# Kernel tuning notes

Hardware: AMD Instinct MI355X
Metric: run time of the kernel (lower is better)

Reference implementation:

```python
import jax, jax.numpy as jnp
import numpy as np

B, L = 8, 1024
VOCAB = 5000
DW = 256            # d_word_vec = d_model
H = 3 * DW          # hidden_size = 768
NH, HD = 12, 64     # n_head, d_k
D = NH * HD         # 768 = nhead*head_dim
D_INNER = 3072
N_LAYERS = 2
N_HIDDEN = 1024
N_OUT = 5000
MASK = 0
SCALE = 1.0 / float(np.sqrt(HD))


def _sinusoid(n_pos, d_hid):
    pos = np.arange(n_pos, dtype=np.float64)[:, None]
    hid = np.arange(d_hid)[None, :]
    tab = pos / np.power(10000.0, 2 * (hid // 2) / d_hid)
    tab[:, 0::2] = np.sin(tab[:, 0::2])
    tab[:, 1::2] = np.cos(tab[:, 1::2])
    tab[0] = 0.0  # padding_idx=0
    return jnp.asarray(tab, dtype=jnp.float32)


def _ln(x, g, b, eps=1e-5):
    mu = x.mean(-1, keepdims=True)
    var = ((x - mu) ** 2).mean(-1, keepdims=True)
    return (x - mu) * jax.lax.rsqrt(var + eps) * g + b


def _dense(x, w, b):
    # w: [out, in] (torch Conv 1x1 / Linear convention)
    return jnp.einsum('...i,oi->...o', x, w) + b


def _pwff(x, w1, b1, w2, b2, g, bn):
    out = _dense(jax.nn.relu(_dense(x, w1, b1)), w2, b2)
    return _ln(out + x, g, bn)


def _msa1(x, relay, wq, bq, wk, bk, wv, bv, wo, bo):
    # x: [B, L, H] nodes, relay: [B, H]. Star-Transformer ring attention:
    # window = 3 local neighbors + the relay node (4 keys per query).
    Bx, Lx, _ = x.shape
    q = _dense(x, wq, bq).reshape(Bx, Lx, NH, HD)
    k = _dense(x, wk, bk).reshape(Bx, Lx, NH, HD)
    v = _dense(x, wv, bv).reshape(Bx, Lx, NH, HD)
    kp = jnp.pad(k, ((0, 0), (1, 1), (0, 0), (0, 0)))
    vp = jnp.pad(v, ((0, 0), (1, 1), (0, 0), (0, 0)))
    k_win = jnp.stack([kp[:, u:u + Lx] for u in range(3)], axis=2)  # [B,L,3,NH,HD]
    v_win = jnp.stack([vp[:, u:u + Lx] for u in range(3)], axis=2)
    rk = _dense(relay, wk, bk).reshape(Bx, NH, HD)
    rv = _dense(relay, wv, bv).reshape(Bx, NH, HD)
    s_loc = jnp.einsum('blnh,blwnh->blwn', q, k_win)
    s_rel = jnp.einsum('blnh,bnh->bln', q, rk)
    scores = jnp.concatenate([s_loc, s_rel[:, :, None, :]], axis=2) * SCALE  # [B,L,4,NH]
    a = jax.nn.softmax(scores, axis=2)
    att = jnp.einsum('blwn,blwnh->blnh', a[:, :, :3], v_win) + a[:, :, 3][..., None] * rv[:, None]
    return _dense(att.reshape(Bx, Lx, D), wo, bo)


def _msa2(relay, nodes, smask, wq, bq, wk, bk, wv, bv, wo, bo):
    # Satellite->planet global attention: single query (relay) over [relay; nodes].
    Bx = relay.shape[0]
    y = jnp.concatenate([relay[:, None, :], nodes], axis=1)  # [B, 1+L, H]
    q = _dense(relay, wq, bq).reshape(Bx, NH, HD)
    k = _dense(y, wk, bk).reshape(Bx, -1, NH, HD)
    v = _dense(y, wv, bv).reshape(Bx, -1, NH, HD)
    pre = jnp.einsum('bnh,bsnh->bns', q, k) * SCALE
    pre = jnp.where(smask[:, None, :], -jnp.inf, pre)
    a = jax.nn.softmax(pre, axis=2)
    att = jnp.einsum('bns,bsnh->bnh', a, v).reshape(Bx, D)
    return _dense(att, wo, bo)


def setup_inputs():
    ks = iter(jax.random.split(jax.random.key(0), 40))
    def w(shape):
        return jax.random.normal(next(ks), shape, dtype=jnp.float32) * 0.02
    def z(shape):
        return jnp.zeros(shape, jnp.float32)
    def o(shape):
        return jnp.ones(shape, jnp.float32)
    inp = {}
    inp['src_seq'] = jax.random.randint(next(ks), (B, L, 3), 0, VOCAB, dtype=jnp.int32)
    inp['positions'] = jax.random.randint(next(ks), (B,), 0, L, dtype=jnp.int32)
    inp['emb'] = w((VOCAB, DW))
    inp['pos_table'] = _sinusoid(L, H)
    inp['norm_g'] = o((N_LAYERS, H)); inp['norm_b'] = z((N_LAYERS, H))
    inp['pw_w1'] = w((N_LAYERS, D_INNER, H)); inp['pw_b1'] = z((N_LAYERS, D_INNER))
    inp['pw_w2'] = w((N_LAYERS, H, D_INNER)); inp['pw_b2'] = z((N_LAYERS, H))
    inp['pw_g'] = o((N_LAYERS, H)); inp['pw_bn'] = z((N_LAYERS, H))
    for p in ['ring', 'star']:
        inp[p + '_wq'] = w((N_LAYERS, D, H)); inp[p + '_bq'] = z((N_LAYERS, D))
        inp[p + '_wk'] = w((N_LAYERS, D, H)); inp[p + '_bk'] = z((N_LAYERS, D))
        inp[p + '_wv'] = w((N_LAYERS, D, H)); inp[p + '_bv'] = z((N_LAYERS, D))
        inp[p + '_wo'] = w((N_LAYERS, H, D)); inp[p + '_bo'] = z((N_LAYERS, H))
    inp['head_w1'] = w((3, N_HIDDEN, 2 * H)); inp['head_b1'] = z((3, N_HIDDEN))
    inp['head_w2'] = w((3, N_OUT, N_HIDDEN)); inp['head_b2'] = z((3, N_OUT))
    return inp


def reference(src_seq, positions, emb, pos_table, norm_g, norm_b, pw_w1, pw_b1, pw_w2, pw_b2, pw_g, pw_bn, ring_wq, ring_bq, ring_wk, ring_bk, ring_wv, ring_bv, ring_wo, ring_bo, star_wq, star_bq, star_wk, star_bk, star_wv, star_bv, star_wo, star_bo, head_w1, head_b1, head_w2, head_b2):
    Bx, Lx, _ = src_seq.shape
    # [B,L,3,DW] -> [B,L,H], add (frozen) sinusoid positional encoding
    x = emb[src_seq].reshape(Bx, Lx, H) + pos_table[None, :Lx]
    mask_pad = src_seq[:, :, 0] == MASK               # True at padded positions
    smask = jnp.concatenate([jnp.zeros((Bx, 1), bool), mask_pad], axis=1)
    nodes = x
    relay = x.mean(axis=1)                            # [B, H]
    for i in range(N_LAYERS):
        h = _pwff(nodes, pw_w1[i], pw_b1[i], pw_w2[i], pw_b2[i], pw_g[i], pw_bn[i])
        ring = _msa1(h, relay, ring_wq[i], ring_bq[i], ring_wk[i], ring_bk[i], ring_wv[i], ring_bv[i], ring_wo[i], ring_bo[i])
        nodes = jax.nn.leaky_relu(_ln(ring, norm_g[i], norm_b[i]))
        relay = jax.nn.leaky_relu(_msa2(relay, nodes, smask, star_wq[i], star_bq[i], star_wk[i], star_bk[i], star_wv[i], star_bv[i], star_wo[i], star_bo[i]))
        nodes = jnp.where(mask_pad[:, :, None], 0.0, nodes)
    target = nodes[jnp.arange(Bx), positions]         # [B, H]
    ft = jnp.concatenate([relay, target], axis=1)     # [B, 2H]
    outs = [_dense(jax.nn.relu(_dense(ft, head_w1[j], head_b1[j])), head_w2[j], head_b2[j]) for j in range(3)]
    return jnp.concatenate(outs, axis=1).reshape(3 * Bx, N_OUT)
```

## Files before the change

kernel.cpp:

```cpp
#include <hip/hip_runtime.h>
#include <cstdint>
#include <cstddef>


typedef unsigned short u16;
typedef __attribute__((ext_vector_type(4))) float f32x4;
typedef __attribute__((ext_vector_type(8))) __bf16 bf16x8;

#define NB 8
#define SEQ 1024
#define HDIM 768
#define NHEAD 12
#define HD 64
#define DINNER 3072
#define NHID 1024
#define NOUT 5000
#define ATT_SCALE 0.125f

static __device__ __forceinline__ float b2f(u16 u) {
  union { float f; uint32_t i; } v; v.i = ((uint32_t)u) << 16; return v.f;
}
static __device__ __forceinline__ u16 f2b(float f) {
  union { float f; uint32_t i; } v; v.f = f;
  uint32_t r = v.i + 0x7fffu + ((v.i >> 16) & 1u);
  return (u16)(r >> 16);
}
static __device__ __forceinline__ float2 b2f2(uint32_t u) {
  union { float f; uint32_t i; } lo, hi;
  lo.i = u << 16; hi.i = u & 0xffff0000u;
  return make_float2(lo.f, hi.f);
}

static __device__ __forceinline__ void gl2lds16(const void* g, void* l) {
  __builtin_amdgcn_global_load_lds(
      (__attribute__((address_space(1))) void*)(uintptr_t)g,
      (__attribute__((address_space(3))) void*)l, 16, 0, 0);
}

template <int N>
static __device__ __forceinline__ void wait_vmcnt() {
  if constexpr (N == 0) asm volatile("s_waitcnt vmcnt(0)" ::: "memory");
  else if constexpr (N == 3) asm volatile("s_waitcnt vmcnt(3)" ::: "memory");
  else if constexpr (N == 4) asm volatile("s_waitcnt vmcnt(4)" ::: "memory");
  else if constexpr (N == 6) asm volatile("s_waitcnt vmcnt(6)" ::: "memory");
  else if constexpr (N == 8) asm volatile("s_waitcnt vmcnt(8)" ::: "memory");
}

static __device__ __forceinline__ float blk_sum(float v, float* red) {
  #pragma unroll
  for (int off = 32; off > 0; off >>= 1) v += __shfl_down(v, off, 64);
  if ((threadIdx.x & 63) == 0) red[threadIdx.x >> 6] = v;
  __syncthreads();
  float r = red[0] + red[1] + red[2] + red[3];
  __syncthreads();
  return r;
}
static __device__ __forceinline__ float blk_max(float v, float* red) {
  #pragma unroll
  for (int off = 32; off > 0; off >>= 1) v = fmaxf(v, __shfl_down(v, off, 64));
  if ((threadIdx.x & 63) == 0) red[threadIdx.x >> 6] = v;
  __syncthreads();
  float r = fmaxf(fmaxf(red[0], red[1]), fmaxf(red[2], red[3]));
  __syncthreads();
  return r;
}

struct Cvt4 {
  const float* s0; const float* s1; const float* s2; const float* s3;
  u16* d0; u16* d1; u16* d2; u16* d3;
  int c1, c2, c3, c4;
};
__global__ __launch_bounds__(256) void cvt4_k(Cvt4 a) {
  const int i = blockIdx.x * 256 + threadIdx.x;
  if (i >= a.c4) return;
  const float* s; u16* d; int j;
  if (i < a.c1)      { s = a.s0; d = a.d0; j = i; }
  else if (i < a.c2) { s = a.s1; d = a.d1; j = i - a.c1; }
  else if (i < a.c3) { s = a.s2; d = a.d2; j = i - a.c2; }
  else               { s = a.s3; d = a.d3; j = i - a.c3; }
  const float4 v = ((const float4*)s)[j];
  ushort4 o;
  o.x = f2b(v.x); o.y = f2b(v.y); o.z = f2b(v.z); o.w = f2b(v.w);
  ((ushort4*)d)[j] = o;
}

template <int ACT, int TM>
__global__ __launch_bounds__(256) void gemm_bt(
    const u16* __restrict__ A,
    const u16* W0, const u16* W1, const u16* W2,
    const float* b0, const float* b1, const float* b2,
    u16* C0, u16* C1, u16* C2,
    int M, int N, int K) {
  constexpr int MI = TM / 32;
  constexpr int S = TM / 64 + 2;
  __shared__ u16 As[4][TM * 32];
  __shared__ u16 Bs[4][128 * 32];
  const int z = blockIdx.z;
  const u16* W = z == 0 ? W0 : (z == 1 ? W1 : W2);
  const float* bias = z == 0 ? b0 : (z == 1 ? b1 : b2);
  u16* C = z == 0 ? C0 : (z == 1 ? C1 : C2);

  const int tid  = threadIdx.x;
  const int wave = tid >> 6;
  const int lane = tid & 63;
  const int bm = blockIdx.y * TM;
  const int bn = blockIdx.x * 128;
  const int wrq = wave >> 1, wcq = wave & 1;
  const int r16 = lane & 15, quad = lane >> 4;
  const int srow = lane >> 2;
  const int scol = (lane & 3) << 3;

  f32x4 acc[MI][4] = {};

  const int nk = K >> 5;

  auto STAGE = [&](int s, int t) {
    const int k0 = t << 5;
    #pragma unroll
    for (int q = 0; q < TM / 64; ++q) {
      const int rowa = wave * (TM / 4) + q * 16;
      gl2lds16(A + (size_t)(bm + rowa + srow) * K + (k0 + scol),
               (char*)&As[s][0] + (rowa << 6));
    }
    #pragma unroll
    for (int q = 0; q < 2; ++q) {
      const int rowb = wave * 32 + q * 16;
      gl2lds16(W + (size_t)(bn + rowb + srow) * K + (k0 + scol),
               (char*)&Bs[s][0] + (rowb << 6));
    }
  };

  STAGE(0, 0);
  if (1 < nk) STAGE(1, 1);

  for (int t = 0; t < nk; ++t) {
    const int s = t & 3;
    if (t + 2 < nk) {
      STAGE((t + 2) & 3, t + 2);
      __builtin_amdgcn_sched_barrier(0);
      wait_vmcnt<2 * S>();
    } else if (t + 1 < nk) {
      wait_vmcnt<S>();
    } else {
      wait_vmcnt<0>();
    }
    __builtin_amdgcn_sched_barrier(0);
    __builtin_amdgcn_s_barrier();
    __builtin_amdgcn_sched_barrier(0);

    bf16x8 af[MI], bf[4];
    #pragma unroll
    for (int i = 0; i < MI; ++i)
      af[i] = *reinterpret_cast<const bf16x8*>(
          &As[s][(wrq * (TM / 2) + i * 16 + r16) * 32 + quad * 8]);
    #pragma unroll
    for (int j = 0; j < 4; ++j)
      bf[j] = *reinterpret_cast<const bf16x8*>(
          &Bs[s][(wcq * 64 + j * 16 + r16) * 32 + quad * 8]);
    #pragma unroll
    for (int i = 0; i < MI; ++i)
      #pragma unroll
      for (int j = 0; j < 4; ++j)
        acc[i][j] = __builtin_amdgcn_mfma_f32_16x16x32_bf16(af[i], bf[j], acc[i][j], 0, 0, 0);
  }

  #pragma unroll
  for (int j = 0; j < 4; ++j) {
    const int n = bn + wcq * 64 + j * 16 + r16;
    const float bv = bias[n];
    #pragma unroll
    for (int i = 0; i < MI; ++i) {
      const int m0 = bm + wrq * (TM / 2) + i * 16 + quad * 4;
      #pragma unroll
      for (int r = 0; r < 4; ++r) {
        float vv = acc[i][j][r] + bv;
        if (ACT == 1) vv = fmaxf(vv, 0.0f);
        C[(size_t)(m0 + r) * N + n] = f2b(vv);
      }
    }
  }
}

__global__ __launch_bounds__(256) void embed_k(
    const int* __restrict__ src, const float* __restrict__ emb,
    const float* __restrict__ pt, float* __restrict__ x,
    u16* __restrict__ xb) {
  const int r = blockIdx.x;
  const int l = r & (SEQ - 1);
  const int tid = threadIdx.x;
  #pragma unroll
  for (int it = 0; it < 3; ++it) {
    const int idx = tid + it * 256;
    const int c = idx >> 8, d = idx & 255;
    const int tok = src[r * 3 + c];
    const float v = emb[(size_t)tok * 256 + d] + pt[(size_t)l * HDIM + idx];
    x[(size_t)r * HDIM + idx] = v;
    xb[(size_t)r * HDIM + idx] = f2b(v);
  }
}

__global__ __launch_bounds__(256) void relay_mean1_k(
    const float* __restrict__ x, float* __restrict__ part) {
  const int cg = blockIdx.x, seg = blockIdx.y, b = blockIdx.z;
  const int h = cg * 256 + threadIdx.x;
  float s = 0.f;
  const int l0 = seg * 64;
  for (int l = l0; l < l0 + 64; ++l) s += x[((size_t)b * SEQ + l) * HDIM + h];
  part[((size_t)b * 16 + seg) * HDIM + h] = s;
}
__global__ __launch_bounds__(256) void relay_mean2_k(
    const float* __restrict__ part, float* __restrict__ relay) {
  const int b = blockIdx.y;
  const int h = blockIdx.x * 256 + threadIdx.x;
  float s = 0.f;
  #pragma unroll
  for (int i = 0; i < 16; ++i) s += part[((size_t)b * 16 + i) * HDIM + h];
  relay[b * HDIM + h] = s * (1.0f / 1024.0f);
}

__global__ __launch_bounds__(256) void ln_resid_k(
    const u16* __restrict__ pre, const float* __restrict__ res,
    const float* __restrict__ g, const float* __restrict__ bb,
    u16* __restrict__ out) {
  __shared__ float red[4];
  const int r = blockIdx.x;
  const int tid = threadIdx.x;
  const size_t base = (size_t)r * HDIM;
  float v0 = b2f(pre[base + tid])       + res[base + tid];
  float v1 = b2f(pre[base + tid + 256]) + res[base + tid + 256];
  float v2 = b2f(pre[base + tid + 512]) + res[base + tid + 512];
  const float mu = blk_sum(v0 + v1 + v2, red) * (1.0f / 768.0f);
  v0 -= mu; v1 -= mu; v2 -= mu;
  const float var = blk_sum(v0 * v0 + v1 * v1 + v2 * v2, red) * (1.0f / 768.0f);
  const float rs = rsqrtf(var + 1e-5f);
  out[base + tid]       = f2b(v0 * rs * g[tid]       + bb[tid]);
  out[base + tid + 256] = f2b(v1 * rs * g[tid + 256] + bb[tid + 256]);
  out[base + tid + 512] = f2b(v2 * rs * g[tid + 512] + bb[tid + 512]);
}

__global__ __launch_bounds__(256) void ln_leaky_mask_k(
    const u16* __restrict__ pre, const float* __restrict__ g,
    const float* __restrict__ bb, const int* __restrict__ src,
    float* __restrict__ out, u16* __restrict__ outb) {
  __shared__ float red[4];
  const int r = blockIdx.x;
  const int tid = threadIdx.x;
  const size_t base = (size_t)r * HDIM;
  float v0 = b2f(pre[base + tid]);
  float v1 = b2f(pre[base + tid + 256]);
  float v2 = b2f(pre[base + tid + 512]);
  const float mu = blk_sum(v0 + v1 + v2, red) * (1.0f / 768.0f);
  v0 -= mu; v1 -= mu; v2 -= mu;
  const float var = blk_sum(v0 * v0 + v1 * v1 + v2 * v2, red) * (1.0f / 768.0f);
  const float rs = rsqrtf(var + 1e-5f);
  const bool masked = (src[r * 3] == 0);
  float y0 = v0 * rs * g[tid]       + bb[tid];
  float y1 = v1 * rs * g[tid + 256] + bb[tid + 256];
  float y2 = v2 * rs * g[tid + 512] + bb[tid + 512];
  y0 = y0 > 0.f ? y0 : 0.01f * y0;
  y1 = y1 > 0.f ? y1 : 0.01f * y1;
  y2 = y2 > 0.f ? y2 : 0.01f * y2;
  if (masked) { y0 = 0.f; y1 = 0.f; y2 = 0.f; }
  out[base + tid]       = y0;  outb[base + tid]       = f2b(y0);
  out[base + tid + 256] = y1;  outb[base + tid + 256] = f2b(y1);
  out[base + tid + 512] = y2;  outb[base + tid + 512] = f2b(y2);
}

__global__ __launch_bounds__(256) void ring_attn_k(
    const u16* __restrict__ q, const u16* __restrict__ k,
    const u16* __restrict__ v, const float* __restrict__ rk,
    const float* __restrict__ rv, u16* __restrict__ att) {
  __shared__ float qs[HDIM];
  __shared__ float aw[NHEAD][4];
  const int r = blockIdx.x;
  const int b = r >> 10, l = r & (SEQ - 1);
  const int tid = threadIdx.x;
  const size_t base = (size_t)r * HDIM;
  #pragma unroll
  for (int it = 0; it < 3; ++it) {
    const int idx = tid + it * 256;
    qs[idx] = b2f(q[base + idx]);
  }
  __syncthreads();
  if (tid < 192) {
    const int u_ = tid >> 2;
    const int l4 = tid & 3;
    const int n = u_ >> 2, w = u_ & 3;
    const float* qrow = qs + n * HD + l4 * 16;
    float a = 0.f;
    if (w < 3) {
      const int ll = l - 1 + w;
      if (ll >= 0 && ll < SEQ) {
        const uint4* kp4 =
            (const uint4*)(k + base + (size_t)(w - 1) * HDIM + n * HD + l4 * 16);
        #pragma unroll
        for (int t = 0; t < 2; ++t) {
          const uint4 u = kp4[t];
          const float2 f0 = b2f2(u.x), f1 = b2f2(u.y);
          const float2 f2_ = b2f2(u.z), f3 = b2f2(u.w);
          const float* q8 = qrow + t * 8;
          a += q8[0] * f0.x + q8[1] * f0.y + q8[2] * f1.x + q8[3] * f1.y
             + q8[4] * f2_.x + q8[5] * f2_.y + q8[6] * f3.x + q8[7] * f3.y;
        }
      }
    } else {
      const float4* kp4 = (const float4*)(rk + b * HDIM + n * HD + l4 * 16);
      #pragma unroll
      for (int t = 0; t < 4; ++t) {
        const float4 kv = kp4[t];
        const float* q4 = qrow + t * 4;
        a += q4[0] * kv.x + q4[1] * kv.y + q4[2] * kv.z + q4[3] * kv.w;
      }
    }
    a += __shfl_xor(a, 1, 4);
    a += __shfl_xor(a, 2, 4);
    if (l4 == 0) aw[n][w] = a * ATT_SCALE;
  }
  __syncthreads();
  if (tid < NHEAD) {
    const float s0 = aw[tid][0], s1 = aw[tid][1], s2 = aw[tid][2], s3 = aw[tid][3];
    const float m = fmaxf(fmaxf(s0, s1), fmaxf(s2, s3));
    const float e0 = __expf(s0 - m), e1 = __expf(s1 - m);
    const float e2 = __expf(s2 - m), e3 = __expf(s3 - m);
    const float inv = 1.0f / (e0 + e1 + e2 + e3);
    aw[tid][0] = e0 * inv; aw[tid][1] = e1 * inv;
    aw[tid][2] = e2 * inv; aw[tid][3] = e3 * inv;
  }
  __syncthreads();
  #pragma unroll
  for (int it = 0; it < 3; ++it) {
    const int idx = tid + it * 256;
    const int n = idx >> 6;
    float acc = aw[n][3] * rv[b * HDIM + idx];
    if (l > 0)       acc += aw[n][0] * b2f(v[base - HDIM + idx]);
    acc += aw[n][1] * b2f(v[base + idx]);
    if (l < SEQ - 1) acc += aw[n][2] * b2f(v[base + HDIM + idx]);
    att[base + idx] = f2b(acc);
  }
}

__global__ __launch_bounds__(256) void msa2_attn_k(
    const float* __restrict__ q2, const float* __restrict__ rk2,
    const float* __restrict__ rv2, const u16* __restrict__ k2,
    const u16* __restrict__ v2, const int* __restrict__ src,
    float* __restrict__ att) {
  __shared__ float qs[HD];
  __shared__ float sc[SEQ + 1];
  __shared__ float red[4];
  __shared__ float vred[4][HD];
  const int bid = blockIdx.x;
  const int b = bid / NHEAD, n = bid % NHEAD;
  const int tid = threadIdx.x;
  const int hb = b * HDIM + n * HD;
  if (tid < HD) qs[tid] = q2[hb + tid];
  __syncthreads();
  float lmax = -1e30f;
  for (int s = tid; s <= SEQ; s += 256) {
    float sco;
    if (s == 0) {
      float a = 0.f;
      #pragma unroll
      for (int d = 0; d < HD; ++d) a += qs[d] * rk2[hb + d];
      sco = a * ATT_SCALE;
    } else {
      const int l = s - 1;
      if (src[(b * SEQ + l) * 3] == 0) {
        sco = -1e30f;
      } else {
        const uint4* kp4 =
            (const uint4*)(k2 + ((size_t)b * SEQ + l) * HDIM + n * HD);
        float a = 0.f;
        #pragma unroll
        for (int t = 0; t < 8; ++t) {
          const uint4 u = kp4[t];
          const float2 f0 = b2f2(u.x), f1 = b2f2(u.y);
          const float2 f2_ = b2f2(u.z), f3 = b2f2(u.w);
          const float* q8 = qs + t * 8;
          a += q8[0] * f0.x + q8[1] * f0.y + q8[2] * f1.x + q8[3] * f1.y
             + q8[4] * f2_.x + q8[5] * f2_.y + q8[6] * f3.x + q8[7] * f3.y;
        }
        sco = a * ATT_SCALE;
      }
    }
    sc[s] = sco;
    lmax = fmaxf(lmax, sco);
  }
  lmax = blk_max(lmax, red);
  float lsum = 0.f;
  for (int s = tid; s <= SEQ; s += 256) {
    const float e = __expf(sc[s] - lmax);
    sc[s] = e;
    lsum += e;
  }
  lsum = blk_sum(lsum, red);
  {
    const int dd = tid & 63, grp = tid >> 6;
    float acc = 0.f;
    const u16* vp = v2 + (size_t)b * SEQ * HDIM + n * HD + dd;
    for (int l = grp; l < SEQ; l += 4)
      acc += sc[l + 1] * b2f(vp[(size_t)l * HDIM]);
    vred[grp][dd] = acc;
  }
  __syncthreads();
  if (tid < HD) {
    const float inv = 1.0f / lsum;
    const float a = sc[0] * rv2[hb + tid]
                  + vred[0][tid] + vred[1][tid] + vred[2][tid] + vred[3][tid];
    att[hb + tid] = a * inv;
  }
}

__global__ __launch_bounds__(256) void relay_proj_k(
    const float* __restrict__ A, int N, int nm,
    const float* W0, const float* W1, const float* W2,
    const float* b0, const float* b1, const float* b2v,
    float* O0, float* O1, float* O2, int act) {
  const int wid = blockIdx.x * 4 + (threadIdx.x >> 6);
  const int lane = threadIdx.x & 63;
  const int mat = wid / N, n = wid % N;
  const float* W  = mat == 0 ? W0 : (mat == 1 ? W1 : W2);
  const float* bb = mat == 0 ? b0 : (mat == 1 ? b1 : b2v);
  float* O        = mat == 0 ? O0 : (mat == 1 ? O1 : O2);
  const float4* wr = (const float4*)(W + (size_t)n * HDIM);
  float acc[NB] = {};
  #pragma unroll
  for (int it = 0; it < 3; ++it) {
    const int k4 = it * 64 + lane;
    const float4 wv = wr[k4];
    #pragma unroll
    for (int b = 0; b < NB; ++b) {
      const float4 av = *(const float4*)&A[b * HDIM + k4 * 4];
      acc[b] += av.x * wv.x + av.y * wv.y + av.z * wv.z + av.w * wv.w;
    }
  }
  #pragma unroll
  for (int b = 0; b < NB; ++b) {
    float a = acc[b];
    #pragma unroll
    for (int off = 32; off > 0; off >>= 1) a += __shfl_down(a, off, 64);
    if (lane == 0) {
      float v = a + bb[n];
      if (act == 2) v = v > 0.f ? v : 0.01f * v;
      O[(size_t)b * N + n] = v;
    }
  }
}

__global__ __launch_bounds__(256) void ft_k(
    const float* __restrict__ relay, const float* __restrict__ nodes,
    const int* __restrict__ positions, float* __restrict__ ft) {
  const int gid = blockIdx.x * 256 + threadIdx.x;
  const int b = gid / 1536, j = gid % 1536;
  if (j < HDIM) {
    ft[gid] = relay[b * HDIM + j];
  } else {
    const int p = positions[b];
    ft[gid] = nodes[((size_t)b * SEQ + p) * HDIM + (j - HDIM)];
  }
}

__global__ __launch_bounds__(256) void head1_k(
    const float* __restrict__ ft, const float* __restrict__ w,
    const float* __restrict__ bias, float* __restrict__ hid) {
  __shared__ float fs[NB * 1536];
  const int j = blockIdx.y;
  {
    const float4* s4 = (const float4*)ft;
    float4* d4 = (float4*)fs;
    for (int i = threadIdx.x; i < (NB * 1536) / 4; i += 256) d4[i] = s4[i];
  }
  __syncthreads();
  const int wave = threadIdx.x >> 6, lane = threadIdx.x & 63;
  const int o = blockIdx.x * 4 + wave;
  const float4* wr = (const float4*)(w + ((size_t)j * NHID + o) * 1536);
  float acc[NB] = {};
  #pragma unroll
  for (int it = 0; it < 6; ++it) {
    const int k4 = it * 64 + lane;
    const float4 wv = wr[k4];
    #pragma unroll
    for (int b = 0; b < NB; ++b) {
      const float4 hv = *(const float4*)&fs[b * 1536 + k4 * 4];
      acc[b] += hv.x * wv.x + hv.y * wv.y + hv.z * wv.z + hv.w * wv.w;
    }
  }
  #pragma unroll
  for (int b = 0; b < NB; ++b) {
    float a = acc[b];
    #pragma unroll
    for (int off = 32; off > 0; off >>= 1) a += __shfl_down(a, off, 64);
    if (lane == 0)
      hid[((size_t)j * NB + b) * NHID + o] = fmaxf(a + bias[j * NHID + o], 0.f);
  }
}

__global__ __launch_bounds__(256) void head2_k(
    const float* __restrict__ hid, const float* __restrict__ w,
    const float* __restrict__ bias, float* __restrict__ out) {
  __shared__ float hs[NB * NHID];
  const int j = blockIdx.y;
  {
    const float4* s4 = (const float4*)(hid + (size_t)j * NB * NHID);
    float4* d4 = (float4*)hs;
    for (int i = threadIdx.x; i < (NB * NHID) / 4; i += 256) d4[i] = s4[i];
  }
  __syncthreads();
  const int wave = threadIdx.x >> 6, lane = threadIdx.x & 63;
  const int o = blockIdx.x * 4 + wave;
  const float4* wr = (const float4*)(w + ((size_t)j * NOUT + o) * NHID);
  float acc[NB] = {};
  #pragma unroll
  for (int it = 0; it < 4; ++it) {
    const int k4 = it * 64 + lane;
    const float4 wv = wr[k4];
    #pragma unroll
    for (int b = 0; b < NB; ++b) {
      const float4 hv = *(const float4*)&hs[b * NHID + k4 * 4];
      acc[b] += hv.x * wv.x + hv.y * wv.y + hv.z * wv.z + hv.w * wv.w;
    }
  }
  #pragma unroll
  for (int b = 0; b < NB; ++b) {
    float a = acc[b];
    #pragma unroll
    for (int off = 32; off > 0; off >>= 1) a += __shfl_down(a, off, 64);
    if (lane == 0)
      out[(size_t)(b * 3 + j) * NOUT + o] = a + bias[j * NOUT + o];
  }
}

extern "C" void kernel_launch(void* const* d_in, const int* in_sizes, int n_in,
                              void* d_out, int out_size, void* d_ws, size_t ws_size,
                              hipStream_t stream) {
  (void)in_sizes; (void)n_in; (void)out_size; (void)ws_size;
  const int* src       = (const int*)d_in[0];
  const int* positions = (const int*)d_in[1];
  const float* emb   = (const float*)d_in[2];
  const float* pt    = (const float*)d_in[3];
  const float* norm_g = (const float*)d_in[4]; const float* norm_b = (const float*)d_in[5];
  const float* pw_w1 = (const float*)d_in[6];  const float* pw_b1 = (const float*)d_in[7];
  const float* pw_w2 = (const float*)d_in[8];  const float* pw_b2 = (const float*)d_in[9];
  const float* pw_g  = (const float*)d_in[10]; const float* pw_bn = (const float*)d_in[11];
  const float* ring_wq = (const float*)d_in[12]; const float* ring_bq = (const float*)d_in[13];
  const float* ring_wk = (const float*)d_in[14]; const float* ring_bk = (const float*)d_in[15];
  const float* ring_wv = (const float*)d_in[16]; const float* ring_bv = (const float*)d_in[17];
  const float* ring_wo = (const float*)d_in[18]; const float* ring_bo = (const float*)d_in[19];
  const float* star_wq = (const float*)d_in[20]; const float* star_bq = (const float*)d_in[21];
  const float* star_wk = (const float*)d_in[22]; const float* star_bk = (const float*)d_in[23];
  const float* star_wv = (const float*)d_in[24]; const float* star_bv = (const float*)d_in[25];
  const float* star_wo = (const float*)d_in[26]; const float* star_bo = (const float*)d_in[27];
  const float* head_w1 = (const float*)d_in[28]; const float* head_b1 = (const float*)d_in[29];
  const float* head_w2 = (const float*)d_in[30]; const float* head_b2 = (const float*)d_in[31];

  char* ws = (char*)d_ws;
  const size_t NTOK = (size_t)NB * SEQ * HDIM;
  float* nodes   = (float*)(ws);
  u16* preln     = (u16*)(ws + NTOK * 4);
  u16* cbase     = (u16*)(ws + NTOK * 6);
  u16* inner  = cbase;
  u16* slotC0 = cbase;
  u16* slotC1 = cbase + 1 * NTOK;
  u16* slotC2 = cbase + 2 * NTOK;
  u16* slotC3 = cbase + 3 * NTOK;
  u16* shared12  = (u16*)(ws + NTOK * 14);
  u16* wc        = (u16*)(ws + NTOK * 16);
  char* small    = ws + NTOK * 16 + 9437184;
  float* part  = (float*)(small);
  float* relay = (float*)(small + 393216);
  float* sb0 = (float*)(small + 393216 + 1 * 24576);
  float* sb1 = (float*)(small + 393216 + 2 * 24576);
  float* sb2 = (float*)(small + 393216 + 3 * 24576);
  float* sb3 = (float*)(small + 393216 + 4 * 24576);
  float* ftb = (float*)(small + 393216 + 5 * 24576);
  float* hid = (float*)(small + 393216 + 5 * 24576 + 49152);

  u16* nodes_b16 = shared12;
  u16* hbuf      = shared12;

  embed_k<<<NB * SEQ, 256, 0, stream>>>(src, emb, pt, nodes, nodes_b16);
  relay_mean1_k<<<dim3(3, 16, NB), 256, 0, stream>>>(nodes, part);
  relay_mean2_k<<<dim3(3, NB), 256, 0, stream>>>(part, relay);

  const int NW1 = DINNER * HDIM;
  const int NQK = HDIM * HDIM;

  for (int i = 0; i < 2; ++i) {
    const float* pw_w1_l = pw_w1 + (size_t)i * NW1;
    const float* pw_w2_l = pw_w2 + (size_t)i * NW1;
    const float* pw_b1_l = pw_b1 + (size_t)i * DINNER;
    const float* pw_b2_l = pw_b2 + (size_t)i * HDIM;
    const float* pw_g_l  = pw_g + (size_t)i * HDIM;
    const float* pw_bn_l = pw_bn + (size_t)i * HDIM;
    const float* ng_l = norm_g + (size_t)i * HDIM;
    const float* nb_l = norm_b + (size_t)i * HDIM;
    const float* rwq = ring_wq + (size_t)i * NQK; const float* rbq = ring_bq + (size_t)i * HDIM;
    const float* rwk = ring_wk + (size_t)i * NQK; const float* rbk = ring_bk + (size_t)i * HDIM;
    const float* rwv = ring_wv + (size_t)i * NQK; const float* rbv = ring_bv + (size_t)i * HDIM;
    const float* rwo = ring_wo + (size_t)i * NQK; const float* rbo = ring_bo + (size_t)i * HDIM;
    const float* swq = star_wq + (size_t)i * NQK; const float* sbq = star_bq + (size_t)i * HDIM;
    const float* swk = star_wk + (size_t)i * NQK; const float* sbk = star_bk + (size_t)i * HDIM;
    const float* swv = star_wv + (size_t)i * NQK; const float* sbv = star_bv + (size_t)i * HDIM;
    const float* swo = star_wo + (size_t)i * NQK; const float* sbo = star_bo + (size_t)i * HDIM;

    u16* wc_pw1 = wc;
    u16* wc_pw2 = wc + NW1;
    {
      Cvt4 a = { pw_w1_l, pw_w2_l, pw_w1_l, pw_w1_l,
                 wc_pw1, wc_pw2, wc_pw1, wc_pw1,
                 NW1 / 4, NW1 / 2, NW1 / 2, NW1 / 2 };
      cvt4_k<<<(NW1 / 2 + 255) / 256, 256, 0, stream>>>(a);
    }
    gemm_bt<1, 128><<<dim3(DINNER / 128, 64, 1), 256, 0, stream>>>(
        nodes_b16, wc_pw1, wc_pw1, wc_pw1, pw_b1_l, pw_b1_l, pw_b1_l,
        inner, inner, inner, NB * SEQ, DINNER, HDIM);
    gemm_bt<0, 64><<<dim3(HDIM / 128, 128, 1), 256, 0, stream>>>(
        inner, wc_pw2, wc_pw2, wc_pw2, pw_b2_l, pw_b2_l, pw_b2_l,
        preln, preln, preln, NB * SEQ, HDIM, DINNER);
    ln_resid_k<<<NB * SEQ, 256, 0, stream>>>(preln, nodes, pw_g_l, pw_bn_l, hbuf);

    u16* wc_rq = wc;
    u16* wc_rk = wc + NQK;
    u16* wc_rv = wc + 2 * NQK;
    u16* wc_ro = wc + 3 * NQK;
    {
      Cvt4 a = { rwq, rwk, rwv, rwo, wc_rq, wc_rk, wc_rv, wc_ro,
                 NQK / 4, NQK / 2, 3 * NQK / 4, NQK };
      cvt4_k<<<(NQK + 255) / 256, 256, 0, stream>>>(a);
    }
    gemm_bt<0, 64><<<dim3(HDIM / 128, 128, 3), 256, 0, stream>>>(
        hbuf, wc_rq, wc_rk, wc_rv, rbq, rbk, rbv,
        slotC0, slotC1, slotC2, NB * SEQ, HDIM, HDIM);
    relay_proj_k<<<2 * HDIM / 4, 256, 0, stream>>>(
        relay, HDIM, 2, rwk, rwv, rwk, rbk, rbv, rbk, sb0, sb1, sb2, 0);
    ring_attn_k<<<NB * SEQ, 256, 0, stream>>>(slotC0, slotC1, slotC2, sb0, sb1, slotC3);
    gemm_bt<0, 64><<<dim3(HDIM / 128, 128, 1), 256, 0, stream>>>(
        slotC3, wc_ro, wc_ro, wc_ro, rbo, rbo, rbo,
        preln, preln, preln, NB * SEQ, HDIM, HDIM);
    ln_leaky_mask_k<<<NB * SEQ, 256, 0, stream>>>(preln, ng_l, nb_l, src, nodes, nodes_b16);

    u16* wc_sk = wc;
    u16* wc_sv = wc + NQK;
    {
      Cvt4 a = { swk, swv, swk, swk, wc_sk, wc_sv, wc_sk, wc_sk,
                 NQK / 4, NQK / 2, NQK / 2, NQK / 2 };
      cvt4_k<<<(NQK / 2 + 255) / 256, 256, 0, stream>>>(a);
    }
    gemm_bt<0, 64><<<dim3(HDIM / 128, 128, 2), 256, 0, stream>>>(
        nodes_b16, wc_sk, wc_sv, wc_sv, sbk, sbv, sbv,
        slotC0, slotC1, slotC1, NB * SEQ, HDIM, HDIM);
    relay_proj_k<<<3 * HDIM / 4, 256, 0, stream>>>(
        relay, HDIM, 3, swq, swk, swv, sbq, sbk, sbv, sb0, sb1, sb2, 0);
    msa2_attn_k<<<NB * NHEAD, 256, 0, stream>>>(sb0, sb1, sb2, slotC0, slotC1, src, sb3);
    relay_proj_k<<<HDIM / 4, 256, 0, stream>>>(
        sb3, HDIM, 1, swo, swo, swo, sbo, sbo, sbo, relay, sb1, sb2, 2);
  }

  ft_k<<<48, 256, 0, stream>>>(relay, nodes, positions, ftb);
  head1_k<<<dim3(NHID / 4, 3), 256, 0, stream>>>(ftb, head_w1, head_b1, hid);
  head2_k<<<dim3(NOUT / 4, 3), 256, 0, stream>>>(hid, head_w2, head_b2, (float*)d_out);
}
```

Baseline: 1.087 ms.

## Flatten GEMM matrix index into grid x, simplify attention dot loops, relayout workspace

The multi-matrix GEMM now folds the matrix selector into blockIdx.x instead of blockIdx.z, which changes block scheduling order. Ring and star attention drop the vectorized uint4 loads and quad-lane shuffle reductions in favour of scalar per-element loops. The star attention value reduction moves from all 256 threads to only 64. The workspace is also reassigned into separate buffers. The simpler attention code uses far fewer threads and narrower loads, so those kernels risk becoming slower.

```diff
diff --git a/kernel.cpp b/kernel.cpp
--- a/kernel.cpp
+++ b/kernel.cpp
@@ -24,11 +24,6 @@
   union { float f; uint32_t i; } v; v.f = f;
   uint32_t r = v.i + 0x7fffu + ((v.i >> 16) & 1u);
   return (u16)(r >> 16);
-}
-static __device__ __forceinline__ float2 b2f2(uint32_t u) {
-  union { float f; uint32_t i; } lo, hi;
-  lo.i = u << 16; hi.i = u & 0xffff0000u;
-  return make_float2(lo.f, hi.f);
 }
 
 static __device__ __forceinline__ void gl2lds16(const void* g, void* l) {
@@ -95,16 +90,17 @@
   constexpr int S = TM / 64 + 2;
   __shared__ u16 As[4][TM * 32];
   __shared__ u16 Bs[4][128 * 32];
-  const int z = blockIdx.z;
-  const u16* W = z == 0 ? W0 : (z == 1 ? W1 : W2);
-  const float* bias = z == 0 ? b0 : (z == 1 ? b1 : b2);
-  u16* C = z == 0 ? C0 : (z == 1 ? C1 : C2);
+  const int nblk = N >> 7;
+  const int mat = (int)blockIdx.x / nblk;
+  const u16* W = mat == 0 ? W0 : (mat == 1 ? W1 : W2);
+  const float* bias = mat == 0 ? b0 : (mat == 1 ? b1 : b2);
+  u16* C = mat == 0 ? C0 : (mat == 1 ? C1 : C2);
 
   const int tid  = threadIdx.x;
   const int wave = tid >> 6;
   const int lane = tid & 63;
   const int bm = blockIdx.y * TM;
-  const int bn = blockIdx.x * 128;
+  const int bn = ((int)blockIdx.x - mat * nblk) * 128;
   const int wrq = wave >> 1, wcq = wave & 1;
   const int r16 = lane & 15, quad = lane >> 4;
   const int srow = lane >> 2;
@@ -282,39 +278,22 @@
     qs[idx] = b2f(q[base + idx]);
   }
   __syncthreads();
-  if (tid < 192) {
-    const int u_ = tid >> 2;
-    const int l4 = tid & 3;
-    const int n = u_ >> 2, w = u_ & 3;
-    const float* qrow = qs + n * HD + l4 * 16;
+  if (tid < NHEAD * 4) {
+    const int n = tid >> 2, w = tid & 3;
     float a = 0.f;
     if (w < 3) {
       const int ll = l - 1 + w;
       if (ll >= 0 && ll < SEQ) {
-        const uint4* kp4 =
-            (const uint4*)(k + base + (size_t)(w - 1) * HDIM + n * HD + l4 * 16);
+        const u16* kp = k + base + (size_t)(w - 1) * HDIM + n * HD;
         #pragma unroll
-        for (int t = 0; t < 2; ++t) {
-          const uint4 u = kp4[t];
-          const float2 f0 = b2f2(u.x), f1 = b2f2(u.y);
-          const float2 f2_ = b2f2(u.z), f3 = b2f2(u.w);
-          const float* q8 = qrow + t * 8;
-          a += q8[0] * f0.x + q8[1] * f0.y + q8[2] * f1.x + q8[3] * f1.y
-             + q8[4] * f2_.x + q8[5] * f2_.y + q8[6] * f3.x + q8[7] * f3.y;
-        }
+        for (int d = 0; d < HD; ++d) a += qs[n * HD + d] * b2f(kp[d]);
       }
     } else {
-      const float4* kp4 = (const float4*)(rk + b * HDIM + n * HD + l4 * 16);
+      const float* kp = rk + b * HDIM + n * HD;
       #pragma unroll
-      for (int t = 0; t < 4; ++t) {
-        const float4 kv = kp4[t];
-        const float* q4 = qrow + t * 4;
-        a += q4[0] * kv.x + q4[1] * kv.y + q4[2] * kv.z + q4[3] * kv.w;
-      }
-    }
-    a += __shfl_xor(a, 1, 4);
-    a += __shfl_xor(a, 2, 4);
-    if (l4 == 0) aw[n][w] = a * ATT_SCALE;
+      for (int d = 0; d < HD; ++d) a += qs[n * HD + d] * kp[d];
+    }
+    aw[n][w] = a * ATT_SCALE;
   }
   __syncthreads();
   if (tid < NHEAD) {
@@ -347,7 +326,6 @@
   __shared__ float qs[HD];
   __shared__ float sc[SEQ + 1];
   __shared__ float red[4];
-  __shared__ float vred[4][HD];
   const int bid = blockIdx.x;
   const int b = bid / NHEAD, n = bid % NHEAD;
   const int tid = threadIdx.x;
@@ -367,18 +345,10 @@
       if (src[(b * SEQ + l) * 3] == 0) {
         sco = -1e30f;
       } else {
-        const uint4* kp4 =
-            (const uint4*)(k2 + ((size_t)b * SEQ + l) * HDIM + n * HD);
+        const u16* kp = k2 + ((size_t)b * SEQ + l) * HDIM + n * HD;
         float a = 0.f;
         #pragma unroll
-        for (int t = 0; t < 8; ++t) {
-          const uint4 u = kp4[t];
-          const float2 f0 = b2f2(u.x), f1 = b2f2(u.y);
-          const float2 f2_ = b2f2(u.z), f3 = b2f2(u.w);
-          const float* q8 = qs + t * 8;
-          a += q8[0] * f0.x + q8[1] * f0.y + q8[2] * f1.x + q8[3] * f1.y
-             + q8[4] * f2_.x + q8[5] * f2_.y + q8[6] * f3.x + q8[7] * f3.y;
-        }
+        for (int d = 0; d < HD; ++d) a += qs[d] * b2f(kp[d]);
         sco = a * ATT_SCALE;
       }
     }
@@ -393,20 +363,12 @@
     lsum += e;
   }
   lsum = blk_sum(lsum, red);
-  {
-    const int dd = tid & 63, grp = tid >> 6;
-    float acc = 0.f;
-    const u16* vp = v2 + (size_t)b * SEQ * HDIM + n * HD + dd;
-    for (int l = grp; l < SEQ; l += 4)
-      acc += sc[l + 1] * b2f(vp[(size_t)l * HDIM]);
-    vred[grp][dd] = acc;
-  }
-  __syncthreads();
   if (tid < HD) {
     const float inv = 1.0f / lsum;
-    const float a = sc[0] * rv2[hb + tid]
-                  + vred[0][tid] + vred[1][tid] + vred[2][tid] + vred[3][tid];
-    att[hb + tid] = a * inv;
+    float acc = sc[0] * rv2[hb + tid];
+    const u16* vp = v2 + (size_t)b * SEQ * HDIM + n * HD + tid;
+    for (int l = 0; l < SEQ; ++l) acc += sc[l + 1] * b2f(vp[(size_t)l * HDIM]);
+    att[hb + tid] = acc * inv;
   }
 }
 
@@ -554,17 +516,21 @@
 
   char* ws = (char*)d_ws;
   const size_t NTOK = (size_t)NB * SEQ * HDIM;
+  const size_t U = NTOK * 2;
   float* nodes   = (float*)(ws);
-  u16* preln     = (u16*)(ws + NTOK * 4);
-  u16* cbase     = (u16*)(ws + NTOK * 6);
-  u16* inner  = cbase;
-  u16* slotC0 = cbase;
-  u16* slotC1 = cbase + 1 * NTOK;
-  u16* slotC2 = cbase + 2 * NTOK;
-  u16* slotC3 = cbase + 3 * NTOK;
-  u16* shared12  = (u16*)(ws + NTOK * 14);
-  u16* wc        = (u16*)(ws + NTOK * 16);
-  char* small    = ws + NTOK * 16 + 9437184;
+  u16* inner     = (u16*)(ws + 2 * U);
+  u16* prelnA    = (u16*)(ws + 6 * U);
+  u16* hbuf      = (u16*)(ws + 2 * U);
+  u16* qb        = (u16*)(ws + 3 * U);
+  u16* kb        = (u16*)(ws + 4 * U);
+  u16* vb        = (u16*)(ws + 5 * U);
+  u16* attb      = (u16*)(ws + 6 * U);
+  u16* prelnB    = (u16*)(ws + 3 * U);
+  u16* nodes_b16 = (u16*)(ws + 7 * U);
+  u16* k2b       = (u16*)(ws + 4 * U);
+  u16* v2b       = (u16*)(ws + 5 * U);
+  u16* wc        = (u16*)(ws + 8 * U);
+  char* small    = ws + 8 * U + 9437184;
   float* part  = (float*)(small);
   float* relay = (float*)(small + 393216);
   float* sb0 = (float*)(small + 393216 + 1 * 24576);
@@ -574,15 +540,13 @@
   float* ftb = (float*)(small + 393216 + 5 * 24576);
   float* hid = (float*)(small + 393216 + 5 * 24576 + 49152);
 
-  u16* nodes_b16 = shared12;
-  u16* hbuf      = shared12;
-
   embed_k<<<NB * SEQ, 256, 0, stream>>>(src, emb, pt, nodes, nodes_b16);
   relay_mean1_k<<<dim3(3, 16, NB), 256, 0, stream>>>(nodes, part);
   relay_mean2_k<<<dim3(3, NB), 256, 0, stream>>>(part, relay);
 
   const int NW1 = DINNER * HDIM;
   const int NQK = HDIM * HDIM;
+  const int M = NB * SEQ;
 
   for (int i = 0; i < 2; ++i) {
     const float* pw_w1_l = pw_w1 + (size_t)i * NW1;
@@ -610,13 +574,13 @@
                  NW1 / 4, NW1 / 2, NW1 / 2, NW1 / 2 };
       cvt4_k<<<(NW1 / 2 + 255) / 256, 256, 0, stream>>>(a);
     }
-    gemm_bt<1, 128><<<dim3(DINNER / 128, 64, 1), 256, 0, stream>>>(
+    gemm_bt<1, 128><<<dim3(DINNER / 128, M / 128), 256, 0, stream>>>(
         nodes_b16, wc_pw1, wc_pw1, wc_pw1, pw_b1_l, pw_b1_l, pw_b1_l,
-        inner, inner, inner, NB * SEQ, DINNER, HDIM);
-    gemm_bt<0, 64><<<dim3(HDIM / 128, 128, 1), 256, 0, stream>>>(
+        inner, inner, inner, M, DINNER, HDIM);
+    gemm_bt<0, 64><<<dim3(HDIM / 128, M / 64), 256, 0, stream>>>(
         inner, wc_pw2, wc_pw2, wc_pw2, pw_b2_l, pw_b2_l, pw_b2_l,
-        preln, preln, preln, NB * SEQ, HDIM, DINNER);
-    ln_resid_k<<<NB * SEQ, 256, 0, stream>>>(preln, nodes, pw_g_l, pw_bn_l, hbuf);
+        prelnA, prelnA, prelnA, M, HDIM, DINNER);
+    ln_resid_k<<<M, 256, 0, stream>>>(prelnA, nodes, pw_g_l, pw_bn_l, hbuf);
 
     u16* wc_rq = wc;
     u16* wc_rk = wc + NQK;
@@ -627,16 +591,16 @@
                  NQK / 4, NQK / 2, 3 * NQK / 4, NQK };
       cvt4_k<<<(NQK + 255) / 256, 256, 0, stream>>>(a);
     }
-    gemm_bt<0, 64><<<dim3(HDIM / 128, 128, 3), 256, 0, stream>>>(
+    gemm_bt<0, 64><<<dim3(3 * (HDIM / 128), M / 64), 256, 0, stream>>>(
         hbuf, wc_rq, wc_rk, wc_rv, rbq, rbk, rbv,
-        slotC0, slotC1, slotC2, NB * SEQ, HDIM, HDIM);
+        qb, kb, vb, M, HDIM, HDIM);
     relay_proj_k<<<2 * HDIM / 4, 256, 0, stream>>>(
         relay, HDIM, 2, rwk, rwv, rwk, rbk, rbv, rbk, sb0, sb1, sb2, 0);
-    ring_attn_k<<<NB * SEQ, 256, 0, stream>>>(slotC0, slotC1, slotC2, sb0, sb1, slotC3);
-    gemm_bt<0, 64><<<dim3(HDIM / 128, 128, 1), 256, 0, stream>>>(
-        slotC3, wc_ro, wc_ro, wc_ro, rbo, rbo, rbo,
-        preln, preln, preln, NB * SEQ, HDIM, HDIM);
-    ln_leaky_mask_k<<<NB * SEQ, 256, 0, stream>>>(preln, ng_l, nb_l, src, nodes, nodes_b16);
+    ring_attn_k<<<NB * SEQ, 256, 0, stream>>>(qb, kb, vb, sb0, sb1, attb);
+    gemm_bt<0, 64><<<dim3(HDIM / 128, M / 64), 256, 0, stream>>>(
+        attb, wc_ro, wc_ro, wc_ro, rbo, rbo, rbo,
+        prelnB, prelnB, prelnB, M, HDIM, HDIM);
+    ln_leaky_mask_k<<<M, 256, 0, stream>>>(prelnB, ng_l, nb_l, src, nodes, nodes_b16);
 
     u16* wc_sk = wc;
     u16* wc_sv = wc + NQK;
@@ -645,12 +609,12 @@
                  NQK / 4, NQK / 2, NQK / 2, NQK / 2 };
       cvt4_k<<<(NQK / 2 + 255) / 256, 256, 0, stream>>>(a);
     }
-    gemm_bt<0, 64><<<dim3(HDIM / 128, 128, 2), 256, 0, stream>>>(
+    gemm_bt<0, 64><<<dim3(2 * (HDIM / 128), M / 64), 256, 0, stream>>>(
         nodes_b16, wc_sk, wc_sv, wc_sv, sbk, sbv, sbv,
-        slotC0, slotC1, slotC1, NB * SEQ, HDIM, HDIM);
+        k2b, v2b, v2b, M, HDIM, HDIM);
     relay_proj_k<<<3 * HDIM / 4, 256, 0, stream>>>(
         relay, HDIM, 3, swq, swk, swv, sbq, sbk, sbv, sb0, sb1, sb2, 0);
-    msa2_attn_k<<<NB * NHEAD, 256, 0, stream>>>(sb0, sb1, sb2, slotC0, slotC1, src, sb3);
+    msa2_attn_k<<<NB * NHEAD, 256, 0, stream>>>(sb0, sb1, sb2, k2b, v2b, src, sb3);
     relay_proj_k<<<HDIM / 4, 256, 0, stream>>>(
         sb3, HDIM, 1, swo, swo, swo, sbo, sbo, sbo, relay, sb1, sb2, 2);
   }
```

Measured after the change: 1.059 ms. 2.6% less time.
